# Kernel tuning notes

Measured on AMD Instinct MI355X. Metric: run time of the kernel, lower is better.

Reference implementation:

```python
import jax, jax.numpy as jnp
import numpy as np


def _lstm_layer(x_seq, h0, c0, Wih, Whh, bih, bhh):
    """Standard (PyTorch-gate-order: i, f, g, o) LSTM over a [T, B, C] sequence."""
    b = bih + bhh  # [4H]
    # Precompute input projections for all timesteps at once: [T, B, 4H]
    x_proj = jnp.einsum('tbc,gc->tbg', x_seq, Wih) + b

    def step(carry, xp_t):
        h, c = carry
        gates = xp_t + h @ Whh.T  # [B, 4H]
        i, f, g, o = jnp.split(gates, 4, axis=-1)
        i = jax.nn.sigmoid(i)
        f = jax.nn.sigmoid(f)
        g = jnp.tanh(g)
        o = jax.nn.sigmoid(o)
        c_new = f * c + i * g
        h_new = o * jnp.tanh(c_new)
        return (h_new, c_new), h_new

    (hT, cT), ys = jax.lax.scan(step, (h0, c0), x_proj)
    return ys, hT, cT


def setup_inputs() -> dict:
    key = jax.random.key(0)
    ks = jax.random.split(key, 16)
    T, B, C, H = 1024, 64, 256, 512
    s_in = 1.0 / np.sqrt(H)
    inp = {
        'x': jax.random.normal(ks[0], (T, B, C), jnp.float32),
        'h0_0': jax.random.normal(ks[1], (B, H), jnp.float32) * 0.1,
        'c0_0': jax.random.normal(ks[2], (B, H), jnp.float32) * 0.1,
        'h0_1': jax.random.normal(ks[3], (B, H), jnp.float32) * 0.1,
        'c0_1': jax.random.normal(ks[4], (B, H), jnp.float32) * 0.1,
        'Wih0': jax.random.normal(ks[5], (4 * H, C), jnp.float32) * s_in,
        'Whh0': jax.random.normal(ks[6], (4 * H, H), jnp.float32) * s_in,
        'bih0': jax.random.normal(ks[7], (4 * H,), jnp.float32) * s_in,
        'bhh0': jax.random.normal(ks[8], (4 * H,), jnp.float32) * s_in,
        'Wih1': jax.random.normal(ks[9], (4 * H, H), jnp.float32) * s_in,
        'Whh1': jax.random.normal(ks[10], (4 * H, H), jnp.float32) * s_in,
        'bih1': jax.random.normal(ks[11], (4 * H,), jnp.float32) * s_in,
        'bhh1': jax.random.normal(ks[12], (4 * H,), jnp.float32) * s_in,
    }
    return inp


def reference(x, h0_0, c0_0, h0_1, c0_1, Wih0, Whh0, bih0, bhh0, Wih1, Whh1, bih1, bhh1):
    # Layer 0 over the full sequence, then layer 1 consumes its outputs.
    # Mathematically identical to the original timestep-major Python loop.
    y0, h1f, c1f = _lstm_layer(x, h0_0, c0_0, Wih0, Whh0, bih0, bhh0)
    y1, h2f, c2f = _lstm_layer(y0, h0_1, c0_1, Wih1, Whh1, bih1, bhh1)
    return (y1, h1f, c1f, h2f, c2f)
```

## Files before the change

### kernel.cpp

```cpp
#include <hip/hip_runtime.h>


#define TT 1024
#define BB 64
#define CC 256
#define HH 512
#define Y_ELEMS (TT * BB * HH)
#define S_ELEMS (BB * HH)
#define RING 4
#define POLL_MAX 8192

typedef __attribute__((ext_vector_type(8))) short bf16x8;
typedef __attribute__((ext_vector_type(4))) float f32x4;
typedef unsigned int u32;
typedef unsigned short u16;
typedef unsigned long long u64;

#define WS_CNT   0
#define WS_BSUM0 4096
#define WS_BSUM1 12288
#define WS_H0R   20480
#define WS_H1R   282624
#define WS_WPK0  413696
#define WS_WPK1  3559424
#define WS_XB    7753728
#define WS_XB_END (WS_XB + (size_t)TT * BB * CC * 2)

__device__ __forceinline__ u16 f2b_rne(float f) {
    u32 u = __float_as_uint(f);
    return (u16)((u + 0x7FFFu + ((u >> 16) & 1u)) >> 16);
}
__device__ __forceinline__ u16 f2b_fast(float f) {
    return (u16)((__float_as_uint(f) + 0x8000u) >> 16);
}
__device__ __forceinline__ float sigf(float z) { return 1.0f / (1.0f + __expf(-z)); }
__device__ __forceinline__ float tanh_f(float z) { return 2.0f / (1.0f + __expf(-2.0f * z)) - 1.0f; }

__device__ __forceinline__ bf16x8 pack8(float4 a, float4 b) {
    union { u16 u[8]; bf16x8 v; } r;
    r.u[0] = f2b_fast(a.x); r.u[1] = f2b_fast(a.y); r.u[2] = f2b_fast(a.z); r.u[3] = f2b_fast(a.w);
    r.u[4] = f2b_fast(b.x); r.u[5] = f2b_fast(b.y); r.u[6] = f2b_fast(b.z); r.u[7] = f2b_fast(b.w);
    return r.v;
}

__device__ __forceinline__ u64 cload64(const u64* p) {
    return __hip_atomic_load((u64*)p, __ATOMIC_RELAXED, __HIP_MEMORY_SCOPE_AGENT);
}
__device__ __forceinline__ u32 cload32(const u32* p) {
    return __hip_atomic_load((u32*)p, __ATOMIC_RELAXED, __HIP_MEMORY_SCOPE_AGENT);
}
__device__ __forceinline__ void cstore64(u64* p, u64 v) {
    __hip_atomic_store(p, v, __ATOMIC_RELAXED, __HIP_MEMORY_SCOPE_AGENT);
}
__device__ __forceinline__ u32 cadd32(u32* p, u32 v) {
    return __hip_atomic_fetch_add(p, v, __ATOMIC_RELAXED, __HIP_MEMORY_SCOPE_AGENT);
}

__device__ __forceinline__ void poll_half(const u32* cnt, int gbase, int lo, u32 needG,
                                          const u32* aux, u32 needAux) {
    const int lane = threadIdx.x & 63;
    const u32* p = (lane >= lo && lane < lo + 4) ? (cnt + (gbase + lane - lo) * 16) : nullptr;
    for (int it = 0; it < POLL_MAX; ++it) {
        int ok = 1;
        if (p) ok = (int)(cload32(p) >= needG);
        if (aux && lane == 8) ok = (int)(cload32(aux) >= needAux);
        if (__ballot(ok) == ~0ull) break;
        __builtin_amdgcn_s_sleep(1);
    }
    asm volatile("" ::: "memory");
}

__device__ __forceinline__ void lds_signal(u32* f, u32 v) {
    __hip_atomic_store(f, v, __ATOMIC_RELEASE, __HIP_MEMORY_SCOPE_WORKGROUP);
}
__device__ __forceinline__ void lds_wait(u32* f, u32 need) {
    for (int it = 0; it < POLL_MAX; ++it) {
        if (__hip_atomic_load(f, __ATOMIC_ACQUIRE, __HIP_MEMORY_SCOPE_WORKGROUP) >= need) break;
        __builtin_amdgcn_s_sleep(0);
    }
    asm volatile("" ::: "memory");
}

__device__ __forceinline__ void publish(u32* cnt, int group, int layerline, u32 t1) {
    u32 prev = cadd32(cnt + group * 16, 1u);
    if (prev == 8u * t1 - 1u) cadd32(cnt + layerline, 1u);
}

__device__ __forceinline__ u64 cell4(const f32x4 g4, float bi, float bf_, float bg_,
                                     float bo, float& c, float& hout) {
    float gi = sigf(g4[0] + bi);
    float gf = sigf(g4[1] + bf_);
    float gc = tanh_f(g4[2] + bg_);
    float go = sigf(g4[3] + bo);
    c = gf * c + gi * gc;
    float h = go * tanh_f(c);
    hout = h;
    const int q = (threadIdx.x & 63) >> 4;
    u32 v = (u32)f2b_rne(h);
    u32 p1 = (u32)__shfl_xor((int)v, 16, 64);
    u32 pair = (q & 1) ? (p1 | (v << 16)) : (v | (p1 << 16));
    u32 p2 = (u32)__shfl_xor((int)pair, 32, 64);
    return (q & 2) ? ((u64)p2 | ((u64)pair << 32)) : ((u64)pair | ((u64)p2 << 32));
}

__global__ void k_init(const float* __restrict__ bih0, const float* __restrict__ bhh0,
                       const float* __restrict__ bih1, const float* __restrict__ bhh1,
                       const float* __restrict__ h00, const float* __restrict__ h01,
                       unsigned char* __restrict__ ws) {
    float* bs0 = (float*)(ws + WS_BSUM0);
    float* bs1 = (float*)(ws + WS_BSUM1);
    u16* h0 = (u16*)(ws + WS_H0R) + (RING - 1) * S_ELEMS;
    u16* h1 = (u16*)(ws + WS_H1R) + S_ELEMS;
    int t = blockIdx.x * 256 + threadIdx.x;
    if (t < 1024) ((u32*)ws)[t] = 0u;
    if (t < 2048) { bs0[t] = bih0[t] + bhh0[t]; bs1[t] = bih1[t] + bhh1[t]; }
    if (t < S_ELEMS) { h0[t] = f2b_rne(h00[t]); h1[t] = f2b_rne(h01[t]); }
}

__global__ void k_xprep(const float* __restrict__ x, unsigned char* __restrict__ ws) {
    u16* xb = (u16*)(ws + WS_XB);
    size_t i = ((size_t)blockIdx.x * 256 + threadIdx.x) * 8;
    float4 f0 = *(const float4*)(x + i);
    float4 f1 = *(const float4*)(x + i + 4);
    *(bf16x8*)(xb + i) = pack8(f0, f1);
}

__global__ void k_wprep(const float* __restrict__ Wih0, const float* __restrict__ Whh0,
                        const float* __restrict__ Wih1, const float* __restrict__ Whh1,
                        unsigned char* __restrict__ ws) {
    u16* wpk0 = (u16*)(ws + WS_WPK0);
    u16* wpk1 = (u16*)(ws + WS_WPK1);
    int u = blockIdx.x * 256 + threadIdx.x;
    const float* s;
    u16* d;
    if (u < 128 * 24 * 64) {
        int cg = u / (24 * 64);
        int kt = (u >> 6) % 24;
        int lane = u & 63;
        int n = lane & 15, quad = lane >> 4;
        int row = (n & 3) * 512 + cg * 4 + (n >> 2);
        int k = kt * 32 + quad * 8;
        s = (k < 256) ? (Wih0 + (size_t)row * 256 + k) : (Whh0 + (size_t)row * 512 + (k - 256));
        d = wpk0 + (size_t)((cg * 24 + kt) * 64 + lane) * 8;
    } else {
        int v = u - 128 * 24 * 64;
        int cg = v / (32 * 64);
        int kt = (v >> 6) % 32;
        int lane = v & 63;
        int n = lane & 15, quad = lane >> 4;
        int row = (n & 3) * 512 + cg * 4 + (n >> 2);
        int k = kt * 32 + quad * 8;
        s = (k < 512) ? (Wih1 + (size_t)row * 512 + k) : (Whh1 + (size_t)row * 512 + (k - 512));
        d = wpk1 + (size_t)((cg * 32 + kt) * 64 + lane) * 8;
    }
    #pragma unroll
    for (int i = 0; i < 8; ++i) d[i] = f2b_rne(s[i]);
}


#define STAGE_HALF_LOAD(dst, srcq, cbase)                                   \
    {                                                                       \
        int row0 = tid >> 5, colu = tid & 31;                               \
        _Pragma("unroll")                                                   \
        for (int i = 0; i < 4; ++i) {                                       \
            int row = i * 8 + row0;                                         \
            dst[2 * i]     = cload64(srcq + row * 128 + (cbase + colu) * 2);\
            dst[2 * i + 1] = cload64(srcq + row * 128 + (cbase + colu) * 2 + 1);\
        }                                                                   \
    }
#define STAGE_HALF_WRITE(sm, src, cbase)                                    \
    {                                                                       \
        int row0 = tid >> 5, colu = tid & 31;                               \
        _Pragma("unroll")                                                   \
        for (int i = 0; i < 4; ++i) {                                       \
            int row = i * 8 + row0;                                         \
            union { u64 q[2]; bf16x8 v; } uu;                               \
            uu.q[0] = src[2 * i]; uu.q[1] = src[2 * i + 1];                 \
            *(bf16x8*)&sm[row * 520 + (cbase + colu) * 8] = uu.v;           \
        }                                                                   \
    }

__device__ void run_l0(const float* __restrict__ x, const float* __restrict__ c0,
                       float* __restrict__ out, unsigned char* __restrict__ ws,
                       int bid, u16* smem, u32* sflag, int use_xb) {
    u32* cnt = (u32*)(ws + WS_CNT);
    const float* bs = (const float*)(ws + WS_BSUM0);
    u16* h0r = (u16*)(ws + WS_H0R);
    const u16* wpk = (const u16*)(ws + WS_WPK0);
    const u16* xb = (const u16*)(ws + WS_XB);

    const int tid = threadIdx.x, lane = tid & 63, wv = tid >> 6;
    const int mg = bid & 1;
    const int cg = (bid >> 1) * 4 + wv;
    const int r16 = lane & 15, quad = lane >> 4, q8 = quad * 8;
    const int col = cg * 4 + quad;

    const float bi = bs[0 * HH + col], bff = bs[1 * HH + col];
    const float bgc = bs[2 * HH + col], bo = bs[3 * HH + col];
    float c[2];
    #pragma unroll
    for (int mt = 0; mt < 2; ++mt)
        c[mt] = c0[(mg * 32 + mt * 16 + r16) * HH + col];

    bf16x8 w[24];
    {
        const u16* wp = wpk + (size_t)(cg * 24 * 64 + lane) * 8;
        #pragma unroll
        for (int kt = 0; kt < 24; ++kt) w[kt] = *(const bf16x8*)(wp + (size_t)kt * 64 * 8);
    }

    for (int t = 0; t < TT; ++t) {
        f32x4 aE[2] = {{0.f,0.f,0.f,0.f},{0.f,0.f,0.f,0.f}};
        f32x4 aO[2] = {{0.f,0.f,0.f,0.f},{0.f,0.f,0.f,0.f}};
        if (use_xb) {
            #pragma unroll
            for (int mt = 0; mt < 2; ++mt) {
                const u16* xp = xb + ((size_t)t * BB + mg * 32 + mt * 16 + r16) * CC + q8;
                #pragma unroll
                for (int kt = 0; kt < 8; ++kt) {
                    bf16x8 a = *(const bf16x8*)(xp + kt * 32);
                    if (kt & 1) aO[mt] = __builtin_amdgcn_mfma_f32_16x16x32_bf16(w[kt], a, aO[mt], 0, 0, 0);
                    else        aE[mt] = __builtin_amdgcn_mfma_f32_16x16x32_bf16(w[kt], a, aE[mt], 0, 0, 0);
                }
            }
        } else {
            #pragma unroll
            for (int mt = 0; mt < 2; ++mt) {
                const float* xp = x + ((size_t)t * BB + mg * 32 + mt * 16 + r16) * CC + q8;
                #pragma unroll
                for (int kt = 0; kt < 8; ++kt) {
                    float4 f0 = *(const float4*)(xp + kt * 32);
                    float4 f1 = *(const float4*)(xp + kt * 32 + 4);
                    bf16x8 a = pack8(f0, f1);
                    if (kt & 1) aO[mt] = __builtin_amdgcn_mfma_f32_16x16x32_bf16(w[kt], a, aO[mt], 0, 0, 0);
                    else        aE[mt] = __builtin_amdgcn_mfma_f32_16x16x32_bf16(w[kt], a, aE[mt], 0, 0, 0);
                }
            }
        }
        const u64* srcq = (const u64*)(h0r + (size_t)((t + RING - 1) & (RING - 1)) * S_ELEMS
                                       + (size_t)mg * 32 * HH);
        u64 sa[8], sb[8];
        if (t) {
            if (wv == 0) {
                const u32* aux = (t >= RING) ? (cnt + 272) : nullptr;
                poll_half(cnt, 0, 0, 8u * (u32)t, aux, 8u * (u32)(t - RING + 1));
                lds_signal(&sflag[0], (u32)t);
            } else lds_wait(&sflag[0], (u32)t);
            STAGE_HALF_LOAD(sa, srcq, 0)
            if (wv == 0) {
                poll_half(cnt, 4, 4, 8u * (u32)t, nullptr, 0u);
                lds_signal(&sflag[1], (u32)t);
            } else lds_wait(&sflag[1], (u32)t);
            STAGE_HALF_WRITE(smem, sa, 0)
            STAGE_HALF_LOAD(sb, srcq, 32)
            STAGE_HALF_WRITE(smem, sb, 32)
        } else {
            STAGE_HALF_LOAD(sa, srcq, 0)
            STAGE_HALF_WRITE(smem, sa, 0)
            STAGE_HALF_LOAD(sb, srcq, 32)
            STAGE_HALF_WRITE(smem, sb, 32)
        }
        __syncthreads();
        #pragma unroll
        for (int kt = 0; kt < 16; ++kt)
            #pragma unroll
            for (int mt = 0; mt < 2; ++mt) {
                bf16x8 a = *(const bf16x8*)&smem[(mt * 16 + r16) * 520 + kt * 32 + q8];
                if (kt & 1) aO[mt] = __builtin_amdgcn_mfma_f32_16x16x32_bf16(w[8 + kt], a, aO[mt], 0, 0, 0);
                else        aE[mt] = __builtin_amdgcn_mfma_f32_16x16x32_bf16(w[8 + kt], a, aE[mt], 0, 0, 0);
            }
        u16* hw = h0r + (size_t)(t & (RING - 1)) * S_ELEMS;
        float hs0, hs1;
        u64 pk0 = cell4(aE[0] + aO[0], bi, bff, bgc, bo, c[0], hs0);
        u64 pk1 = cell4(aE[1] + aO[1], bi, bff, bgc, bo, c[1], hs1);
        if (quad < 2) {
            u64 pk = (quad & 1) ? pk1 : pk0;
            int batch = mg * 32 + quad * 16 + r16;
            cstore64((u64*)(hw + (size_t)batch * HH + cg * 4), pk);
        }
        __syncthreads();
        if (tid == 0) publish(cnt, bid >> 3, 256, (u32)(t + 1));
        if (t == TT - 1) {
            float* fin = out + Y_ELEMS;
            int b0_ = mg * 32 + r16;
            fin[b0_ * HH + col] = hs0;
            fin[S_ELEMS + b0_ * HH + col] = c[0];
            fin[(b0_ + 16) * HH + col] = hs1;
            fin[S_ELEMS + (b0_ + 16) * HH + col] = c[1];
        }
    }
}

__device__ void run_l1(const float* __restrict__ c0, float* __restrict__ out,
                       unsigned char* __restrict__ ws, int b2, u16* smem, u32* sflag) {
    u32* cnt = (u32*)(ws + WS_CNT);
    const float* bs = (const float*)(ws + WS_BSUM1);
    const u16* h0r = (const u16*)(ws + WS_H0R);
    u16* h1r = (u16*)(ws + WS_H1R);
    const u16* wpk = (const u16*)(ws + WS_WPK1);
    const int TILE1 = 32 * 520;

    const int tid = threadIdx.x, lane = tid & 63, wv = tid >> 6;
    const int mg = b2 & 1;
    const int cg = (b2 >> 1) * 4 + wv;
    const int r16 = lane & 15, quad = lane >> 4, q8 = quad * 8;
    const int col = cg * 4 + quad;

    const float bi = bs[0 * HH + col], bff = bs[1 * HH + col];
    const float bgc = bs[2 * HH + col], bo = bs[3 * HH + col];
    float c[2];
    #pragma unroll
    for (int mt = 0; mt < 2; ++mt)
        c[mt] = c0[(mg * 32 + mt * 16 + r16) * HH + col];

    bf16x8 w[32];
    {
        const u16* wp = wpk + (size_t)(cg * 32 * 64 + lane) * 8;
        #pragma unroll
        for (int kt = 0; kt < 32; ++kt) w[kt] = *(const bf16x8*)(wp + (size_t)kt * 64 * 8);
    }

    for (int t = 0; t < TT; ++t) {
        const u64* sy = (const u64*)(h0r + (size_t)(t & (RING - 1)) * S_ELEMS
                                     + (size_t)mg * 32 * HH);
        const u64* sh = (const u64*)(h1r + (size_t)((t + 1) & 1) * S_ELEMS
                                     + (size_t)mg * 32 * HH);
        u64 ya[8], yb[8], hc[16];
        if (wv == 0) {
            poll_half(cnt, 0, 0, 8u * (u32)(t + 1), t ? (cnt + 272) : nullptr, 8u * (u32)t);
            lds_signal(&sflag[0], (u32)(t + 1));
        } else lds_wait(&sflag[0], (u32)(t + 1));
        STAGE_HALF_LOAD(ya, sy, 0)
        #pragma unroll
        for (int i = 0; i < 8; ++i) {
            int ch = i * 256 + tid;
            hc[2 * i]     = cload64(sh + ch * 2);
            hc[2 * i + 1] = cload64(sh + ch * 2 + 1);
        }
        if (wv == 0) {
            poll_half(cnt, 4, 4, 8u * (u32)(t + 1), nullptr, 0u);
            lds_signal(&sflag[1], (u32)(t + 1));
        } else lds_wait(&sflag[1], (u32)(t + 1));
        STAGE_HALF_WRITE(smem, ya, 0)
        STAGE_HALF_LOAD(yb, sy, 32)
        STAGE_HALF_WRITE(smem, yb, 32)
        __syncthreads();
        f32x4 aE[2] = {{0.f,0.f,0.f,0.f},{0.f,0.f,0.f,0.f}};
        f32x4 aO[2] = {{0.f,0.f,0.f,0.f},{0.f,0.f,0.f,0.f}};
        #pragma unroll
        for (int kt = 0; kt < 16; ++kt)
            #pragma unroll
            for (int mt = 0; mt < 2; ++mt) {
                bf16x8 a = *(const bf16x8*)&smem[(mt * 16 + r16) * 520 + kt * 32 + q8];
                if (kt & 1) aO[mt] = __builtin_amdgcn_mfma_f32_16x16x32_bf16(w[kt], a, aO[mt], 0, 0, 0);
                else        aE[mt] = __builtin_amdgcn_mfma_f32_16x16x32_bf16(w[kt], a, aE[mt], 0, 0, 0);
            }
        #pragma unroll
        for (int i = 0; i < 8; ++i) {
            int ch = i * 256 + tid;
            union { u64 q[2]; bf16x8 v; } uu;
            uu.q[0] = hc[2 * i]; uu.q[1] = hc[2 * i + 1];
            *(bf16x8*)&smem[TILE1 + (ch >> 6) * 520 + (ch & 63) * 8] = uu.v;
        }
        __syncthreads();
        #pragma unroll
        for (int kt = 0; kt < 16; ++kt)
            #pragma unroll
            for (int mt = 0; mt < 2; ++mt) {
                bf16x8 a = *(const bf16x8*)&smem[TILE1 + (mt * 16 + r16) * 520 + kt * 32 + q8];
                if (kt & 1) aO[mt] = __builtin_amdgcn_mfma_f32_16x16x32_bf16(w[16 + kt], a, aO[mt], 0, 0, 0);
                else        aE[mt] = __builtin_amdgcn_mfma_f32_16x16x32_bf16(w[16 + kt], a, aE[mt], 0, 0, 0);
            }
        u16* hw = h1r + (size_t)(t & 1) * S_ELEMS;
        float hs0, hs1;
        u64 pk0 = cell4(aE[0] + aO[0], bi, bff, bgc, bo, c[0], hs0);
        u64 pk1 = cell4(aE[1] + aO[1], bi, bff, bgc, bo, c[1], hs1);
        if (quad < 2) {
            u64 pk = (quad & 1) ? pk1 : pk0;
            int batch = mg * 32 + quad * 16 + r16;
            cstore64((u64*)(hw + (size_t)batch * HH + cg * 4), pk);
        }
        __syncthreads();
        if (tid == 0) publish(cnt, 8 + (b2 >> 3), 272, (u32)(t + 1));
        {
            int b0_ = mg * 32 + r16;
            out[(size_t)t * S_ELEMS + b0_ * HH + col] = hs0;
            out[(size_t)t * S_ELEMS + (b0_ + 16) * HH + col] = hs1;
            if (t == TT - 1) {
                float* fin = out + Y_ELEMS + 2 * S_ELEMS;
                fin[b0_ * HH + col] = hs0;
                fin[S_ELEMS + b0_ * HH + col] = c[0];
                fin[(b0_ + 16) * HH + col] = hs1;
                fin[S_ELEMS + (b0_ + 16) * HH + col] = c[1];
            }
        }
    }
}

__global__ __launch_bounds__(256, 1) void k_lstm(const float* __restrict__ x,
                                                 const float* __restrict__ c00,
                                                 const float* __restrict__ c01,
                                                 float* __restrict__ out,
                                                 unsigned char* __restrict__ ws,
                                                 int use_xb) {
    __shared__ __align__(16) u16 smem[2 * 32 * 520];
    __shared__ u32 sflag[2];
    if (threadIdx.x < 2) sflag[threadIdx.x] = 0u;
    __syncthreads();
    const int bid = blockIdx.x;
    if (bid < 64) run_l0(x, c00, out, ws, bid, smem, sflag, use_xb);
    else          run_l1(c01, out, ws, bid - 64, smem, sflag);
}

extern "C" void kernel_launch(void* const* d_in, const int* in_sizes, int n_in,
                              void* d_out, int out_size, void* d_ws, size_t ws_size,
                              hipStream_t stream) {
    const float* x    = (const float*)d_in[0];
    const float* h0_0 = (const float*)d_in[1];
    const float* c0_0 = (const float*)d_in[2];
    const float* h0_1 = (const float*)d_in[3];
    const float* c0_1 = (const float*)d_in[4];
    const float* Wih0 = (const float*)d_in[5];
    const float* Whh0 = (const float*)d_in[6];
    const float* bih0 = (const float*)d_in[7];
    const float* bhh0 = (const float*)d_in[8];
    const float* Wih1 = (const float*)d_in[9];
    const float* Whh1 = (const float*)d_in[10];
    const float* bih1 = (const float*)d_in[11];
    const float* bhh1 = (const float*)d_in[12];
    float* out = (float*)d_out;
    unsigned char* ws = (unsigned char*)d_ws;

    int use_xb = (ws_size >= (size_t)WS_XB_END) ? 1 : 0;
    k_init<<<128, 256, 0, stream>>>(bih0, bhh0, bih1, bhh1, h0_0, h0_1, ws);
    k_wprep<<<1792, 256, 0, stream>>>(Wih0, Whh0, Wih1, Whh1, ws);
    if (use_xb) k_xprep<<<8192, 256, 0, stream>>>(x, ws);
    k_lstm<<<128, 256, 0, stream>>>(x, c0_0, c0_1, out, ws, use_xb);
}
```

Baseline: 5.275 ms.

## Publish per-wave completion and split staging to overlap half-tile MFMA

Each wave now signals completion itself after waiting on its own global stores, instead of a block-wide barrier followed by a single-thread publish. Group counters therefore count waves, so thresholds change from 8 to 32 per step. Staging of the hidden-state tile is split so the first half of the K-loop MFMAs runs before the second half is written to LDS, overlapping loads with compute. This shortens the critical path of the recurrent step, at the cost of an extra barrier and four times more atomics per step.

Measured after the change: 5.749 ms. 1.09x slower.

```diff
diff --git a/kernel.cpp b/kernel.cpp
--- a/kernel.cpp
+++ b/kernel.cpp
@@ -81,9 +81,9 @@
     asm volatile("" ::: "memory");
 }
 
-__device__ __forceinline__ void publish(u32* cnt, int group, int layerline, u32 t1) {
+__device__ __forceinline__ void publishW(u32* cnt, int group, int layerline, u32 t1) {
     u32 prev = cadd32(cnt + group * 16, 1u);
-    if (prev == 8u * t1 - 1u) cadd32(cnt + layerline, 1u);
+    if (prev == 32u * t1 - 1u) cadd32(cnt + layerline, 1u);
 }
 
 __device__ __forceinline__ u64 cell4(const f32x4 g4, float bi, float bf_, float bg_,
@@ -243,26 +243,32 @@
         if (t) {
             if (wv == 0) {
                 const u32* aux = (t >= RING) ? (cnt + 272) : nullptr;
-                poll_half(cnt, 0, 0, 8u * (u32)t, aux, 8u * (u32)(t - RING + 1));
+                poll_half(cnt, 0, 0, 32u * (u32)t, aux, 8u * (u32)(t - RING + 1));
                 lds_signal(&sflag[0], (u32)t);
             } else lds_wait(&sflag[0], (u32)t);
-            STAGE_HALF_LOAD(sa, srcq, 0)
+        }
+        STAGE_HALF_LOAD(sa, srcq, 0)
+        if (t) {
             if (wv == 0) {
-                poll_half(cnt, 4, 4, 8u * (u32)t, nullptr, 0u);
+                poll_half(cnt, 4, 4, 32u * (u32)t, nullptr, 0u);
                 lds_signal(&sflag[1], (u32)t);
             } else lds_wait(&sflag[1], (u32)t);
-            STAGE_HALF_WRITE(smem, sa, 0)
-            STAGE_HALF_LOAD(sb, srcq, 32)
-            STAGE_HALF_WRITE(smem, sb, 32)
-        } else {
-            STAGE_HALF_LOAD(sa, srcq, 0)
-            STAGE_HALF_WRITE(smem, sa, 0)
-            STAGE_HALF_LOAD(sb, srcq, 32)
-            STAGE_HALF_WRITE(smem, sb, 32)
-        }
-        __syncthreads();
-        #pragma unroll
-        for (int kt = 0; kt < 16; ++kt)
+        }
+        STAGE_HALF_WRITE(smem, sa, 0)
+        STAGE_HALF_LOAD(sb, srcq, 32)
+        __syncthreads();
+        #pragma unroll
+        for (int kt = 0; kt < 8; ++kt)
+            #pragma unroll
+            for (int mt = 0; mt < 2; ++mt) {
+                bf16x8 a = *(const bf16x8*)&smem[(mt * 16 + r16) * 520 + kt * 32 + q8];
+                if (kt & 1) aO[mt] = __builtin_amdgcn_mfma_f32_16x16x32_bf16(w[8 + kt], a, aO[mt], 0, 0, 0);
+                else        aE[mt] = __builtin_amdgcn_mfma_f32_16x16x32_bf16(w[8 + kt], a, aE[mt], 0, 0, 0);
+            }
+        STAGE_HALF_WRITE(smem, sb, 32)
+        __syncthreads();
+        #pragma unroll
+        for (int kt = 8; kt < 16; ++kt)
             #pragma unroll
             for (int mt = 0; mt < 2; ++mt) {
                 bf16x8 a = *(const bf16x8*)&smem[(mt * 16 + r16) * 520 + kt * 32 + q8];
@@ -278,8 +284,8 @@
             int batch = mg * 32 + quad * 16 + r16;
             cstore64((u64*)(hw + (size_t)batch * HH + cg * 4), pk);
         }
-        __syncthreads();
-        if (tid == 0) publish(cnt, bid >> 3, 256, (u32)(t + 1));
+        asm volatile("s_waitcnt vmcnt(0)" ::: "memory");
+        if (lane == 0) publishW(cnt, bid >> 3, 256, (u32)(t + 1));
         if (t == TT - 1) {
             float* fin = out + Y_ELEMS;
             int b0_ = mg * 32 + r16;
@@ -288,6 +294,7 @@
             fin[(b0_ + 16) * HH + col] = hs1;
             fin[S_ELEMS + (b0_ + 16) * HH + col] = c[1];
         }
+        __syncthreads();
     }
 }
 
@@ -327,7 +334,7 @@
                                      + (size_t)mg * 32 * HH);
         u64 ya[8], yb[8], hc[16];
         if (wv == 0) {
-            poll_half(cnt, 0, 0, 8u * (u32)(t + 1), t ? (cnt + 272) : nullptr, 8u * (u32)t);
+            poll_half(cnt, 0, 0, 32u * (u32)(t + 1), t ? (cnt + 272) : nullptr, 8u * (u32)t);
             lds_signal(&sflag[0], (u32)(t + 1));
         } else lds_wait(&sflag[0], (u32)(t + 1));
         STAGE_HALF_LOAD(ya, sy, 0)
@@ -338,17 +345,26 @@
             hc[2 * i + 1] = cload64(sh + ch * 2 + 1);
         }
         if (wv == 0) {
-            poll_half(cnt, 4, 4, 8u * (u32)(t + 1), nullptr, 0u);
+            poll_half(cnt, 4, 4, 32u * (u32)(t + 1), nullptr, 0u);
             lds_signal(&sflag[1], (u32)(t + 1));
         } else lds_wait(&sflag[1], (u32)(t + 1));
         STAGE_HALF_WRITE(smem, ya, 0)
         STAGE_HALF_LOAD(yb, sy, 32)
-        STAGE_HALF_WRITE(smem, yb, 32)
         __syncthreads();
         f32x4 aE[2] = {{0.f,0.f,0.f,0.f},{0.f,0.f,0.f,0.f}};
         f32x4 aO[2] = {{0.f,0.f,0.f,0.f},{0.f,0.f,0.f,0.f}};
         #pragma unroll
-        for (int kt = 0; kt < 16; ++kt)
+        for (int kt = 0; kt < 8; ++kt)
+            #pragma unroll
+            for (int mt = 0; mt < 2; ++mt) {
+                bf16x8 a = *(const bf16x8*)&smem[(mt * 16 + r16) * 520 + kt * 32 + q8];
+                if (kt & 1) aO[mt] = __builtin_amdgcn_mfma_f32_16x16x32_bf16(w[kt], a, aO[mt], 0, 0, 0);
+                else        aE[mt] = __builtin_amdgcn_mfma_f32_16x16x32_bf16(w[kt], a, aE[mt], 0, 0, 0);
+            }
+        STAGE_HALF_WRITE(smem, yb, 32)
+        __syncthreads();
+        #pragma unroll
+        for (int kt = 8; kt < 16; ++kt)
             #pragma unroll
             for (int mt = 0; mt < 2; ++mt) {
                 bf16x8 a = *(const bf16x8*)&smem[(mt * 16 + r16) * 520 + kt * 32 + q8];
@@ -380,8 +396,8 @@
             int batch = mg * 32 + quad * 16 + r16;
             cstore64((u64*)(hw + (size_t)batch * HH + cg * 4), pk);
         }
-        __syncthreads();
-        if (tid == 0) publish(cnt, 8 + (b2 >> 3), 272, (u32)(t + 1));
+        asm volatile("s_waitcnt vmcnt(0)" ::: "memory");
+        if (lane == 0) publishW(cnt, 8 + (b2 >> 3), 272, (u32)(t + 1));
         {
             int b0_ = mg * 32 + r16;
             out[(size_t)t * S_ELEMS + b0_ * HH + col] = hs0;
@@ -394,6 +410,7 @@
                 fin[S_ELEMS + (b0_ + 16) * HH + col] = c[1];
             }
         }
+        __syncthreads();
     }
 }
 
```
